# Performance work log

Hardware: AMD Instinct MI355X
Metric: run time of the kernel (lower is better)

Reference implementation:

```python
import jax, jax.numpy as jnp
import numpy as np

N_NODES = 100000

def _sage_conv(x, src, dst, W_l, b_l, W_r):
    # PyG SAGEConv (aggr='mean'): out = lin_l(mean_{j in N(i)} x_j) + lin_r(x_i)
    msg = x[src]                                             # [E, d] gather
    agg = jax.ops.segment_sum(msg, dst, num_segments=N_NODES)  # [N, d]
    deg = jax.ops.segment_sum(jnp.ones((src.shape[0],), x.dtype), dst,
                              num_segments=N_NODES)          # [N]
    mean = agg / jnp.maximum(deg, 1.0)[:, None]
    return mean @ W_l + b_l + x @ W_r

def setup_inputs() -> dict:
    key = jax.random.key(0)
    ks = jax.random.split(key, 8)
    d_in, d_hid, d_out = 128, 128, 64
    E = 1_600_000
    x = jax.random.normal(ks[0], (N_NODES, d_in), dtype=jnp.float32)
    edge_index = jax.random.randint(ks[1], (2, E), 0, N_NODES, dtype=jnp.int64)
    s1 = 1.0 / np.sqrt(d_in)
    s2 = 1.0 / np.sqrt(d_hid)
    return {
        "x": x,
        "W1_l": jax.random.uniform(ks[2], (d_in, d_hid), jnp.float32, -s1, s1),
        "b1":   jnp.zeros((d_hid,), jnp.float32),
        "W1_r": jax.random.uniform(ks[3], (d_in, d_hid), jnp.float32, -s1, s1),
        "W2_l": jax.random.uniform(ks[4], (d_hid, d_out), jnp.float32, -s2, s2),
        "b2":   jnp.zeros((d_out,), jnp.float32),
        "W2_r": jax.random.uniform(ks[5], (d_hid, d_out), jnp.float32, -s2, s2),
        "edge_index": edge_index,
    }

def reference(x, W1_l, b1, W1_r, W2_l, b2, W2_r, edge_index):
    src, dst = edge_index[0], edge_index[1]
    h = _sage_conv(x, src, dst, W1_l, b1, W1_r)
    h = jax.nn.relu(h)
    # dropout is identity in eval mode (p=0.5 train-only); omitted for determinism
    out = _sage_conv(h, src, dst, W2_l, b2, W2_r)
    return out
```

## Files before the change

### kernel.cpp

```cpp
#include <hip/hip_runtime.h>
#include <hip/hip_bf16.h>
#include <cstdint>


typedef __bf16 bf16x8 __attribute__((ext_vector_type(8)));
typedef float f32x4 __attribute__((ext_vector_type(4)));
typedef float f32x2 __attribute__((ext_vector_type(2)));

#define MAXBUCK 400
#define MAXEPT 16
#define HISTB 512
#define P2B 512
#define HSTRIDE 136

__device__ __forceinline__ unsigned short f2bf(float f) {
    union { float f; unsigned int u; } v; v.f = f;
    unsigned int u = v.u;
    unsigned int r = ((u >> 16) & 1u) + 0x7fffu;
    return (unsigned short)((u + r) >> 16);
}

__device__ __forceinline__ f32x2 up2(unsigned int u) {
    uint2 t; t.x = u << 16; t.y = u & 0xffff0000u;
    return __builtin_bit_cast(f32x2, t);
}
__device__ __forceinline__ void accp(const uint4& v, f32x2* a) {
    a[0] += up2(v.x);
    a[1] += up2(v.y);
    a[2] += up2(v.z);
    a[3] += up2(v.w);
}
__device__ __forceinline__ void accpw(const uint4& v, float w, f32x2* a) {
    a[0] += up2(v.x) * w;
    a[1] += up2(v.y) * w;
    a[2] += up2(v.z) * w;
    a[3] += up2(v.w) * w;
}

__device__ __forceinline__ int edge_val(const int* ei32, const long long* ei64,
                                        int is64, size_t idx) {
    return is64 ? (int)ei64[idx] : ei32[idx];
}

__global__ __launch_bounds__(256) void detect_zero(const void* ei, int n_nodes,
                                                   int* flag, int* bucket_cnt) {
    for (int i = threadIdx.x; i < MAXBUCK; i += 256) bucket_cnt[i] = 0;
    if (threadIdx.x == 0) {
        const long long* p = (const long long*)ei;
        int ok = 1;
        for (int i = 0; i < 8; ++i) {
            long long v = p[i];
            if (v < 0 || v >= n_nodes) ok = 0;
        }
        *flag = ok;
    }
}

__global__ __launch_bounds__(256) void prep_kernel(const float* __restrict__ x,
                                                   unsigned short* __restrict__ xb,
                                                   long long n8, int ncvt,
                                                   const float* __restrict__ W1l,
                                                   const float* __restrict__ W1r,
                                                   uint4* __restrict__ w1frag,
                                                   const float* __restrict__ W2l,
                                                   const float* __restrict__ W2r,
                                                   uint4* __restrict__ w2frag,
                                                   const int* ei32, const long long* ei64,
                                                   const int* flag, int E, int nbuck,
                                                   int* bucket_cnt) {
    int b = blockIdx.x;
    if (b < ncvt) {
        long long i = (long long)b * 256 + threadIdx.x;
        if (i >= n8) return;
        const float4* p = (const float4*)(x + i * 8);
        float4 a = p[0], c = p[1];
        uint4 o;
        o.x = (unsigned)f2bf(a.x) | ((unsigned)f2bf(a.y) << 16);
        o.y = (unsigned)f2bf(a.z) | ((unsigned)f2bf(a.w) << 16);
        o.z = (unsigned)f2bf(c.x) | ((unsigned)f2bf(c.y) << 16);
        o.w = (unsigned)f2bf(c.z) | ((unsigned)f2bf(c.w) << 16);
        ((uint4*)(xb))[i] = o;
        return;
    }
    if (b < ncvt + 16) {
        int tid = (b - ncvt) * 256 + threadIdx.x;
        int fi = tid >> 6, lane = tid & 63;
        int ct = fi >> 3, ks = fi & 7;
        int k0 = ks * 32 + (lane >> 4) * 8;
        int n = ct * 16 + (lane & 15);
        unsigned short e[8];
#pragma unroll
        for (int j = 0; j < 8; ++j) {
            int k = k0 + j;
            float v = (k < 128) ? W1l[k * 128 + n] : W1r[(k - 128) * 128 + n];
            e[j] = f2bf(v);
        }
        uint4 o;
        o.x = (unsigned)e[0] | ((unsigned)e[1] << 16);
        o.y = (unsigned)e[2] | ((unsigned)e[3] << 16);
        o.z = (unsigned)e[4] | ((unsigned)e[5] << 16);
        o.w = (unsigned)e[6] | ((unsigned)e[7] << 16);
        w1frag[tid] = o;
        return;
    }
    if (b < ncvt + 16 + 8) {
        int tid = (b - ncvt - 16) * 256 + threadIdx.x;
        int fi = tid >> 6, lane = tid & 63;
        int ct = fi >> 2, ks = fi & 3;
        int k0 = ks * 32 + (lane >> 4) * 8;
        int n = ct * 16 + (lane & 15);
        unsigned short e[8];
#pragma unroll
        for (int j = 0; j < 8; ++j) {
            int k = k0 + j;
            float v = (n < 64) ? W2l[k * 64 + n] : W2r[k * 64 + (n - 64)];
            e[j] = f2bf(v);
        }
        uint4 o;
        o.x = (unsigned)e[0] | ((unsigned)e[1] << 16);
        o.y = (unsigned)e[2] | ((unsigned)e[3] << 16);
        o.z = (unsigned)e[4] | ((unsigned)e[5] << 16);
        o.w = (unsigned)e[6] | ((unsigned)e[7] << 16);
        w2frag[tid] = o;
        return;
    }
    __shared__ int lhist[MAXBUCK];
    for (int i = threadIdx.x; i < nbuck; i += 256) lhist[i] = 0;
    __syncthreads();
    int is64 = *flag;
    int hb = b - (ncvt + 24);
    int stride = HISTB * 256;
    for (int e = hb * 256 + threadIdx.x; e < E; e += stride) {
        int d = edge_val(ei32, ei64, is64, (size_t)E + e);
        atomicAdd(&lhist[d >> 8], 1);
    }
    __syncthreads();
    for (int i = threadIdx.x; i < nbuck; i += 256) {
        int c = lhist[i];
        if (c) atomicAdd(&bucket_cnt[i], c);
    }
}

__global__ __launch_bounds__(256) void bucket_scan(const int* bucket_cnt, int nbuck,
                                                   int* bucket_base, int* bucket_pos) {
    int t = threadIdx.x;
    int i0 = 2 * t, i1 = 2 * t + 1;
    int a0 = (i0 < nbuck) ? bucket_cnt[i0] : 0;
    int a1 = (i1 < nbuck) ? bucket_cnt[i1] : 0;
    int tsum = a0 + a1;
    __shared__ int sc[256];
    sc[t] = tsum;
    __syncthreads();
    for (int o = 1; o < 256; o <<= 1) {
        int x = (t >= o) ? sc[t - o] : 0;
        __syncthreads();
        if (t >= o) sc[t] += x;
        __syncthreads();
    }
    int excl = sc[t] - tsum;
    if (i0 <= nbuck) { bucket_base[i0] = excl; if (i0 < nbuck) bucket_pos[i0] = excl; }
    if (i1 <= nbuck) { bucket_base[i1] = excl + a0; if (i1 < nbuck) bucket_pos[i1] = excl + a0; }
    if (t == 255) bucket_base[nbuck] = sc[255];
}

__global__ __launch_bounds__(256) void pass2_partition(const int* ei32, const long long* ei64,
                                                       const int* flag, int E, int ept,
                                                       int nbuck, int* bucket_pos,
                                                       unsigned* ebuf) {
    __shared__ int lhist[MAXBUCK];
    __shared__ int gbase[MAXBUCK];
    for (int i = threadIdx.x; i < nbuck; i += 256) lhist[i] = 0;
    __syncthreads();
    int is64 = *flag;
    int base_e = blockIdx.x * (ept * 256);
    unsigned ed[MAXEPT];
    int bidx[MAXEPT];
    int slot[MAXEPT];
#pragma unroll 4
    for (int i = 0; i < ept; ++i) {
        int e = base_e + i * 256 + threadIdx.x;
        if (e < E) {
            int s = edge_val(ei32, ei64, is64, (size_t)e);
            int d = edge_val(ei32, ei64, is64, (size_t)E + e);
            ed[i] = ((unsigned)s << 8) | (unsigned)(d & 255);
            bidx[i] = d >> 8;
            slot[i] = atomicAdd(&lhist[d >> 8], 1);
        } else {
            slot[i] = -1;
        }
    }
    __syncthreads();
    for (int i = threadIdx.x; i < nbuck; i += 256) {
        int c = lhist[i];
        gbase[i] = c ? atomicAdd(&bucket_pos[i], c) : 0;
    }
    __syncthreads();
#pragma unroll 4
    for (int i = 0; i < ept; ++i) {
        if (slot[i] >= 0) {
            ebuf[gbase[bidx[i]] + slot[i]] = ed[i];
        }
    }
}

__global__ __launch_bounds__(256) void pass3_finalize(const unsigned* __restrict__ ebuf,
                                                      const int* __restrict__ bucket_base,
                                                      int nbuck, int N, int E,
                                                      int* __restrict__ off,
                                                      int* __restrict__ csr) {
    __shared__ int lcnt[256];
    __shared__ int lexcl[256];
    __shared__ int sc[256];
    int b = blockIdx.x;
    int t = threadIdx.x;
    int d0 = b << 8;
    int nb = N - d0; if (nb > 256) nb = 256;
    int base = bucket_base[b];
    int m = bucket_base[b + 1] - base;

    lcnt[t] = 0;
    __syncthreads();
    for (int j = t; j < m; j += 256) {
        int li = (int)(ebuf[base + j] & 255u);
        atomicAdd(&lcnt[li], 1);
    }
    __syncthreads();
    int v = lcnt[t];
    sc[t] = v;
    __syncthreads();
    for (int o = 1; o < 256; o <<= 1) {
        int x = (t >= o) ? sc[t - o] : 0;
        __syncthreads();
        if (t >= o) sc[t] += x;
        __syncthreads();
    }
    int excl = sc[t] - v;
    lexcl[t] = excl;
    if (t < nb) off[d0 + t] = base + excl;
    if (b == nbuck - 1 && t == 0) off[N] = E;
    lcnt[t] = 0;
    __syncthreads();
    for (int j = t; j < m; j += 256) {
        unsigned ed = ebuf[base + j];
        int li = (int)(ed & 255u);
        int slot = atomicAdd(&lcnt[li], 1);
        csr[base + lexcl[li] + slot] = (int)(ed >> 8);
    }
}

__global__ __launch_bounds__(256) void agg_mean128_bf(const unsigned short* __restrict__ Xb,
                                                      const int* __restrict__ off,
                                                      const int* __restrict__ csr,
                                                      unsigned short* __restrict__ outb,
                                                      int n_nodes) {
    int node = blockIdx.x * 4 + (threadIdx.x >> 6);
    if (node >= n_nodes) return;
    int lane = threadIdx.x & 63;
    int quad = lane >> 4;
    int l16 = lane & 15;
    int s0 = off[node], s1 = off[node + 1];
    int deg = s1 - s0;
    f32x2 A0[4], A1[4];
#pragma unroll
    for (int k = 0; k < 4; ++k) { A0[k] = (f32x2){0.f, 0.f}; A1[k] = (f32x2){0.f, 0.f}; }
    int j = s0;
    for (; j + 8 <= s1; j += 8) {
        int p0 = csr[j + quad];
        int p1 = csr[j + 4 + quad];
        uint4 v0 = ((const uint4*)(Xb + (size_t)p0 * 128))[l16];
        uint4 v1 = ((const uint4*)(Xb + (size_t)p1 * 128))[l16];
        accp(v0, A0);
        accp(v1, A1);
    }
    if (j + 4 <= s1) {
        int p = csr[j + quad];
        uint4 v = ((const uint4*)(Xb + (size_t)p * 128))[l16];
        accp(v, A0);
        j += 4;
    }
    if (j < s1) {
        int jj = j + quad;
        int p = csr[(jj < s1) ? jj : (s1 - 1)];
        float w = (jj < s1) ? 1.0f : 0.0f;
        uint4 v = ((const uint4*)(Xb + (size_t)p * 128))[l16];
        accpw(v, w, A1);
    }
    float r[8];
#pragma unroll
    for (int k = 0; k < 4; ++k) {
        f32x2 s = A0[k] + A1[k];
        r[2 * k] = s.x;
        r[2 * k + 1] = s.y;
    }
#pragma unroll
    for (int k = 0; k < 8; ++k) r[k] += __shfl(r[k], lane ^ 16);
#pragma unroll
    for (int k = 0; k < 8; ++k) r[k] += __shfl(r[k], lane ^ 32);
    float inv = (deg > 0) ? 1.0f / (float)deg : 0.0f;
    if (quad == 0) {
        uint4 o;
        o.x = (unsigned)f2bf(r[0] * inv) | ((unsigned)f2bf(r[1] * inv) << 16);
        o.y = (unsigned)f2bf(r[2] * inv) | ((unsigned)f2bf(r[3] * inv) << 16);
        o.z = (unsigned)f2bf(r[4] * inv) | ((unsigned)f2bf(r[5] * inv) << 16);
        o.w = (unsigned)f2bf(r[6] * inv) | ((unsigned)f2bf(r[7] * inv) << 16);
        ((uint4*)(outb + (size_t)node * 128))[l16] = o;
    }
}

__global__ __launch_bounds__(256) void agg_mean64_bf_ep(const unsigned short* __restrict__ Zb,
                                                        const float* __restrict__ Wadd,
                                                        const int* __restrict__ off,
                                                        const int* __restrict__ csr,
                                                        float* __restrict__ out,
                                                        int n_nodes) {
    int node = blockIdx.x * 4 + (threadIdx.x >> 6);
    if (node >= n_nodes) return;
    int lane = threadIdx.x & 63;
    int oct = lane >> 3;
    int l8 = lane & 7;
    int s0 = off[node], s1 = off[node + 1];
    int deg = s1 - s0;
    f32x2 A0[4], A1[4];
#pragma unroll
    for (int k = 0; k < 4; ++k) { A0[k] = (f32x2){0.f, 0.f}; A1[k] = (f32x2){0.f, 0.f}; }
    int j = s0;
    for (; j + 16 <= s1; j += 16) {
        int p0 = csr[j + oct];
        int p1 = csr[j + 8 + oct];
        uint4 v0 = ((const uint4*)(Zb + (size_t)p0 * 64))[l8];
        uint4 v1 = ((const uint4*)(Zb + (size_t)p1 * 64))[l8];
        accp(v0, A0);
        accp(v1, A1);
    }
    if (j + 8 <= s1) {
        int p = csr[j + oct];
        uint4 v = ((const uint4*)(Zb + (size_t)p * 64))[l8];
        accp(v, A0);
        j += 8;
    }
    if (j < s1) {
        int jj = j + oct;
        int p = csr[(jj < s1) ? jj : (s1 - 1)];
        float w = (jj < s1) ? 1.0f : 0.0f;
        uint4 v = ((const uint4*)(Zb + (size_t)p * 64))[l8];
        accpw(v, w, A1);
    }
    float r[8];
#pragma unroll
    for (int k = 0; k < 4; ++k) {
        f32x2 s = A0[k] + A1[k];
        r[2 * k] = s.x;
        r[2 * k + 1] = s.y;
    }
#pragma unroll
    for (int k = 0; k < 8; ++k) r[k] += __shfl(r[k], lane ^ 8);
#pragma unroll
    for (int k = 0; k < 8; ++k) r[k] += __shfl(r[k], lane ^ 16);
#pragma unroll
    for (int k = 0; k < 8; ++k) r[k] += __shfl(r[k], lane ^ 32);
    float inv = (deg > 0) ? 1.0f / (float)deg : 0.0f;
    if (oct == 0) {
        const float4* wp = (const float4*)(Wadd + (size_t)node * 64 + l8 * 8);
        float4 w0 = wp[0], w1 = wp[1];
        float4 o0, o1;
        o0.x = r[0] * inv + w0.x; o0.y = r[1] * inv + w0.y;
        o0.z = r[2] * inv + w0.z; o0.w = r[3] * inv + w0.w;
        o1.x = r[4] * inv + w1.x; o1.y = r[5] * inv + w1.y;
        o1.z = r[6] * inv + w1.z; o1.w = r[7] * inv + w1.w;
        float4* op = (float4*)(out + (size_t)node * 64 + l8 * 8);
        op[0] = o0; op[1] = o1;
    }
}

__global__ __launch_bounds__(256, 3) void gemm12_mfma(const unsigned short* __restrict__ meanb,
                                                      const unsigned short* __restrict__ xb,
                                                      const uint4* __restrict__ w1frag,
                                                      const uint4* __restrict__ w2frag,
                                                      const float* __restrict__ b1,
                                                      const float* __restrict__ b2,
                                                      unsigned short* __restrict__ z2,
                                                      float* __restrict__ w2out,
                                                      int nrows) {
    __shared__ uint4 sW2[2048];
    __shared__ unsigned short hs[4][16 * HSTRIDE];
    for (int i = threadIdx.x; i < 2048; i += 256) sW2[i] = w2frag[i];
    __syncthreads();
    const int wid = threadIdx.x >> 6, lane = threadIdx.x & 63;
    const int quad = lane >> 4, l16 = lane & 15;
    const int m0 = blockIdx.x * 128 + wid * 32;
    unsigned short* hsw = &hs[wid][0];
    const uint4* w1p = w1frag + lane;

#pragma unroll
    for (int mt = 0; mt < 2; ++mt) {
        int row = m0 + mt * 16 + l16;
        int rowc = (row < nrows) ? row : (nrows - 1);
        const uint4* mrow = (const uint4*)(meanb + (size_t)rowc * 128);
        const uint4* xrow = (const uint4*)(xb + (size_t)rowc * 128);
        bf16x8 af[8];
#pragma unroll
        for (int ks = 0; ks < 4; ++ks) {
            af[ks]     = __builtin_bit_cast(bf16x8, mrow[ks * 4 + quad]);
            af[ks + 4] = __builtin_bit_cast(bf16x8, xrow[ks * 4 + quad]);
        }

#pragma unroll
        for (int ct = 0; ct < 8; ++ct) {
            f32x4 acc = (f32x4){0.f, 0.f, 0.f, 0.f};
#pragma unroll
            for (int ks = 0; ks < 8; ++ks) {
                bf16x8 bf = __builtin_bit_cast(bf16x8, w1p[(ct * 8 + ks) * 64]);
                acc = __builtin_amdgcn_mfma_f32_16x16x32_bf16(af[ks], bf, acc, 0, 0, 0);
            }
            int col = ct * 16 + l16;
            float bb = b1[col];
#pragma unroll
            for (int r = 0; r < 4; ++r) {
                float v = fmaxf(acc[r] + bb, 0.f);
                hs[wid][(quad * 4 + r) * HSTRIDE + col] = f2bf(v);
            }
        }

        bf16x8 af2[4];
#pragma unroll
        for (int ks = 0; ks < 4; ++ks) {
            uint4 t = *(const uint4*)(hsw + l16 * HSTRIDE + ks * 32 + quad * 8);
            af2[ks] = __builtin_bit_cast(bf16x8, t);
        }

#pragma unroll
        for (int ct = 0; ct < 8; ++ct) {
            f32x4 acc = (f32x4){0.f, 0.f, 0.f, 0.f};
#pragma unroll
            for (int ks = 0; ks < 4; ++ks) {
                bf16x8 bf = __builtin_bit_cast(bf16x8, sW2[(ct * 4 + ks) * 64 + lane]);
                acc = __builtin_amdgcn_mfma_f32_16x16x32_bf16(af2[ks], bf, acc, 0, 0, 0);
            }
            int col = ct * 16 + l16;
#pragma unroll
            for (int r = 0; r < 4; ++r) {
                int orow = m0 + mt * 16 + quad * 4 + r;
                if (orow < nrows) {
                    if (col < 64) {
                        z2[(size_t)orow * 64 + col] = f2bf(acc[r]);
                    } else {
                        w2out[(size_t)orow * 64 + (col - 64)] = acc[r] + b2[col - 64];
                    }
                }
            }
        }
    }
}

extern "C" void kernel_launch(void* const* d_in, const int* in_sizes, int n_in,
                              void* d_out, int out_size, void* d_ws, size_t ws_size,
                              hipStream_t stream) {
    const float* x    = (const float*)d_in[0];
    const float* W1_l = (const float*)d_in[1];
    const float* b1   = (const float*)d_in[2];
    const float* W1_r = (const float*)d_in[3];
    const float* W2_l = (const float*)d_in[4];
    const float* b2   = (const float*)d_in[5];
    const float* W2_r = (const float*)d_in[6];
    const void*  ei   = d_in[7];
    float* out = (float*)d_out;

    const int N = in_sizes[0] / 128;
    const int E = in_sizes[7] / 2;
    const int nbuck = (N + 255) >> 8;

    uintptr_t base = (uintptr_t)d_ws;
    int* flag = (int*)base;
    int* bucket_cnt  = (int*)(base + 64);
    int* bucket_base = bucket_cnt + MAXBUCK;
    int* bucket_pos  = bucket_base + MAXBUCK + 1;
    int* off = (int*)(base + 4096 + 3 * MAXBUCK * 4);
    off = (int*)(((uintptr_t)off + 255) & ~(uintptr_t)255);
    int* csr = off + (N + 1);
    uintptr_t p = ((uintptr_t)(csr + E) + 255) & ~(uintptr_t)255;
    unsigned short* xb    = (unsigned short*)p; p += (size_t)N * 128 * 2;
    unsigned short* meanb = (unsigned short*)p; p += (size_t)N * 128 * 2;
    unsigned short* hbr   = (unsigned short*)p; p += (size_t)N * 128 * 2;
    uint4* w1frag = (uint4*)p; p += 4096 * 16;
    uint4* w2frag = (uint4*)p; p += 2048 * 16;
    unsigned* ebuf = (unsigned*)meanb;
    unsigned short* z2 = hbr;
    float* w2 = (float*)xb;

    const int* ei32 = (const int*)ei;
    const long long* ei64 = (const long long*)ei;

    detect_zero<<<1, 256, 0, stream>>>(ei, N, flag, bucket_cnt);

    long long n8 = (long long)N * 128 / 8;
    int ncvt = (int)((n8 + 255) / 256);
    prep_kernel<<<ncvt + 16 + 8 + HISTB, 256, 0, stream>>>(
        x, xb, n8, ncvt, W1_l, W1_r, w1frag, W2_l, W2_r, w2frag,
        ei32, ei64, flag, E, nbuck, bucket_cnt);

    bucket_scan<<<1, 256, 0, stream>>>(bucket_cnt, nbuck, bucket_base, bucket_pos);
    int ept = (E + P2B * 256 - 1) / (P2B * 256);
    pass2_partition<<<P2B, 256, 0, stream>>>(ei32, ei64, flag, E, ept, nbuck,
                                             bucket_pos, ebuf);
    pass3_finalize<<<nbuck, 256, 0, stream>>>(ebuf, bucket_base, nbuck, N, E, off, csr);

    int ablocks = (N + 3) / 4;
    int gblocks = (N + 127) / 128;

    agg_mean128_bf<<<ablocks, 256, 0, stream>>>(xb, off, csr, meanb, N);
    gemm12_mfma<<<gblocks, 256, 0, stream>>>(meanb, xb, w1frag, w2frag, b1, b2,
                                             z2, w2, N);
    agg_mean64_bf_ep<<<ablocks, 256, 0, stream>>>(z2, w2, off, csr, out, N);
}
```

Measured before the change: 319.2 us.

## Store bf16 features in column-slab layout for cache-local layer-1 aggregation

Converts x into eight column slabs of 16 bf16 features per node. The layer-1 mean aggregation then runs slice by slice, each slice being a 3.2MB table that can stay in cache, with two lanes per node. The GEMM reads its A fragments from the slab layout, and w2 gets its own workspace buffer instead of aliasing xb, which is now still needed. The cost is eight passes over the CSR indices and divergent per-node loops, since lanes whose node has a smaller degree sit idle until the wave's largest degree finishes.

```diff
diff --git a/kernel.cpp b/kernel.cpp
--- a/kernel.cpp
+++ b/kernel.cpp
@@ -57,8 +57,8 @@
 }
 
 __global__ __launch_bounds__(256) void prep_kernel(const float* __restrict__ x,
-                                                   unsigned short* __restrict__ xb,
-                                                   long long n8, int ncvt,
+                                                   unsigned short* __restrict__ xslab,
+                                                   int N, int ncvt,
                                                    const float* __restrict__ W1l,
                                                    const float* __restrict__ W1r,
                                                    uint4* __restrict__ w1frag,
@@ -70,16 +70,22 @@
                                                    int* bucket_cnt) {
     int b = blockIdx.x;
     if (b < ncvt) {
-        long long i = (long long)b * 256 + threadIdx.x;
-        if (i >= n8) return;
-        const float4* p = (const float4*)(x + i * 8);
-        float4 a = p[0], c = p[1];
-        uint4 o;
-        o.x = (unsigned)f2bf(a.x) | ((unsigned)f2bf(a.y) << 16);
-        o.y = (unsigned)f2bf(a.z) | ((unsigned)f2bf(a.w) << 16);
-        o.z = (unsigned)f2bf(c.x) | ((unsigned)f2bf(c.y) << 16);
-        o.w = (unsigned)f2bf(c.z) | ((unsigned)f2bf(c.w) << 16);
-        ((uint4*)(xb))[i] = o;
+        int nl = threadIdx.x >> 3, s = threadIdx.x & 7;
+        int node = b * 32 + nl;
+        if (node >= N) return;
+        const float4* px = (const float4*)(x + (size_t)node * 128 + s * 16);
+        float4 a0 = px[0], a1 = px[1], a2 = px[2], a3 = px[3];
+        uint4 o0, o1;
+        o0.x = (unsigned)f2bf(a0.x) | ((unsigned)f2bf(a0.y) << 16);
+        o0.y = (unsigned)f2bf(a0.z) | ((unsigned)f2bf(a0.w) << 16);
+        o0.z = (unsigned)f2bf(a1.x) | ((unsigned)f2bf(a1.y) << 16);
+        o0.w = (unsigned)f2bf(a1.z) | ((unsigned)f2bf(a1.w) << 16);
+        o1.x = (unsigned)f2bf(a2.x) | ((unsigned)f2bf(a2.y) << 16);
+        o1.y = (unsigned)f2bf(a2.z) | ((unsigned)f2bf(a2.w) << 16);
+        o1.z = (unsigned)f2bf(a3.x) | ((unsigned)f2bf(a3.y) << 16);
+        o1.w = (unsigned)f2bf(a3.z) | ((unsigned)f2bf(a3.w) << 16);
+        uint4* dst = (uint4*)(xslab + (size_t)s * N * 16 + (size_t)node * 16);
+        dst[0] = o0; dst[1] = o1;
         return;
     }
     if (b < ncvt + 16) {
@@ -248,62 +254,40 @@
     }
 }
 
-__global__ __launch_bounds__(256) void agg_mean128_bf(const unsigned short* __restrict__ Xb,
-                                                      const int* __restrict__ off,
-                                                      const int* __restrict__ csr,
-                                                      unsigned short* __restrict__ outb,
-                                                      int n_nodes) {
-    int node = blockIdx.x * 4 + (threadIdx.x >> 6);
-    if (node >= n_nodes) return;
-    int lane = threadIdx.x & 63;
-    int quad = lane >> 4;
-    int l16 = lane & 15;
-    int s0 = off[node], s1 = off[node + 1];
-    int deg = s1 - s0;
-    f32x2 A0[4], A1[4];
-#pragma unroll
-    for (int k = 0; k < 4; ++k) { A0[k] = (f32x2){0.f, 0.f}; A1[k] = (f32x2){0.f, 0.f}; }
-    int j = s0;
-    for (; j + 8 <= s1; j += 8) {
-        int p0 = csr[j + quad];
-        int p1 = csr[j + 4 + quad];
-        uint4 v0 = ((const uint4*)(Xb + (size_t)p0 * 128))[l16];
-        uint4 v1 = ((const uint4*)(Xb + (size_t)p1 * 128))[l16];
-        accp(v0, A0);
-        accp(v1, A1);
-    }
-    if (j + 4 <= s1) {
-        int p = csr[j + quad];
-        uint4 v = ((const uint4*)(Xb + (size_t)p * 128))[l16];
-        accp(v, A0);
-        j += 4;
-    }
-    if (j < s1) {
-        int jj = j + quad;
-        int p = csr[(jj < s1) ? jj : (s1 - 1)];
-        float w = (jj < s1) ? 1.0f : 0.0f;
-        uint4 v = ((const uint4*)(Xb + (size_t)p * 128))[l16];
-        accpw(v, w, A1);
-    }
-    float r[8];
-#pragma unroll
-    for (int k = 0; k < 4; ++k) {
-        f32x2 s = A0[k] + A1[k];
-        r[2 * k] = s.x;
-        r[2 * k + 1] = s.y;
-    }
-#pragma unroll
-    for (int k = 0; k < 8; ++k) r[k] += __shfl(r[k], lane ^ 16);
-#pragma unroll
-    for (int k = 0; k < 8; ++k) r[k] += __shfl(r[k], lane ^ 32);
-    float inv = (deg > 0) ? 1.0f / (float)deg : 0.0f;
-    if (quad == 0) {
+__global__ __launch_bounds__(256) void agg_mean128_slab(const unsigned short* __restrict__ xslab,
+                                                        const int* __restrict__ off,
+                                                        const int* __restrict__ csr,
+                                                        unsigned short* __restrict__ meanslab,
+                                                        int N) {
+    int slice = blockIdx.x & 7;
+    int g = blockIdx.x >> 3;
+    int wid = threadIdx.x >> 6, lane = threadIdx.x & 63;
+    int nl = lane >> 1, h = lane & 1;
+    int node = g * 128 + wid * 32 + nl;
+    int valid = node < N;
+    int s0 = 0, deg = 0;
+    if (valid) { s0 = off[node]; deg = off[node + 1] - s0; }
+    const unsigned short* slab = xslab + (size_t)slice * N * 16 + h * 8;
+    f32x2 A[4];
+    A[0] = A[1] = A[2] = A[3] = (f32x2){0.f, 0.f};
+    for (int i = 0; ; ++i) {
+        int act = (i < deg);
+        if (!__any(act)) break;
+        if (act) {
+            int p = csr[s0 + i];
+            uint4 v = *(const uint4*)(slab + (size_t)p * 16);
+            accp(v, A);
+        }
+    }
+    if (valid) {
+        float inv = (deg > 0) ? 1.0f / (float)deg : 0.0f;
+        f32x2 r0 = A[0] * inv, r1 = A[1] * inv, r2 = A[2] * inv, r3 = A[3] * inv;
         uint4 o;
-        o.x = (unsigned)f2bf(r[0] * inv) | ((unsigned)f2bf(r[1] * inv) << 16);
-        o.y = (unsigned)f2bf(r[2] * inv) | ((unsigned)f2bf(r[3] * inv) << 16);
-        o.z = (unsigned)f2bf(r[4] * inv) | ((unsigned)f2bf(r[5] * inv) << 16);
-        o.w = (unsigned)f2bf(r[6] * inv) | ((unsigned)f2bf(r[7] * inv) << 16);
-        ((uint4*)(outb + (size_t)node * 128))[l16] = o;
+        o.x = (unsigned)f2bf(r0.x) | ((unsigned)f2bf(r0.y) << 16);
+        o.y = (unsigned)f2bf(r1.x) | ((unsigned)f2bf(r1.y) << 16);
+        o.z = (unsigned)f2bf(r2.x) | ((unsigned)f2bf(r2.y) << 16);
+        o.w = (unsigned)f2bf(r3.x) | ((unsigned)f2bf(r3.y) << 16);
+        *(uint4*)(meanslab + (size_t)slice * N * 16 + (size_t)node * 16 + h * 8) = o;
     }
 }
 
@@ -372,8 +356,8 @@
     }
 }
 
-__global__ __launch_bounds__(256, 3) void gemm12_mfma(const unsigned short* __restrict__ meanb,
-                                                      const unsigned short* __restrict__ xb,
+__global__ __launch_bounds__(256, 3) void gemm12_mfma(const unsigned short* __restrict__ meanslab,
+                                                      const unsigned short* __restrict__ xslab,
                                                       const uint4* __restrict__ w1frag,
                                                       const uint4* __restrict__ w2frag,
                                                       const float* __restrict__ b1,
@@ -390,18 +374,21 @@
     const int m0 = blockIdx.x * 128 + wid * 32;
     unsigned short* hsw = &hs[wid][0];
     const uint4* w1p = w1frag + lane;
+    const size_t sstride = (size_t)nrows * 16;
+    const int eo = (quad & 1) * 8;
+    const int slq = quad >> 1;
 
 #pragma unroll
     for (int mt = 0; mt < 2; ++mt) {
         int row = m0 + mt * 16 + l16;
         int rowc = (row < nrows) ? row : (nrows - 1);
-        const uint4* mrow = (const uint4*)(meanb + (size_t)rowc * 128);
-        const uint4* xrow = (const uint4*)(xb + (size_t)rowc * 128);
         bf16x8 af[8];
 #pragma unroll
         for (int ks = 0; ks < 4; ++ks) {
-            af[ks]     = __builtin_bit_cast(bf16x8, mrow[ks * 4 + quad]);
-            af[ks + 4] = __builtin_bit_cast(bf16x8, xrow[ks * 4 + quad]);
+            af[ks]     = __builtin_bit_cast(bf16x8,
+                *(const uint4*)(meanslab + (size_t)(2 * ks + slq) * sstride + (size_t)rowc * 16 + eo));
+            af[ks + 4] = __builtin_bit_cast(bf16x8,
+                *(const uint4*)(xslab + (size_t)(2 * ks + slq) * sstride + (size_t)rowc * 16 + eo));
         }
 
 #pragma unroll
@@ -478,24 +465,23 @@
     off = (int*)(((uintptr_t)off + 255) & ~(uintptr_t)255);
     int* csr = off + (N + 1);
     uintptr_t p = ((uintptr_t)(csr + E) + 255) & ~(uintptr_t)255;
-    unsigned short* xb    = (unsigned short*)p; p += (size_t)N * 128 * 2;
-    unsigned short* meanb = (unsigned short*)p; p += (size_t)N * 128 * 2;
-    unsigned short* hbr   = (unsigned short*)p; p += (size_t)N * 128 * 2;
+    unsigned short* xslab    = (unsigned short*)p; p += (size_t)N * 128 * 2;
+    unsigned short* meanslab = (unsigned short*)p; p += (size_t)N * 128 * 2;
+    unsigned short* hbr      = (unsigned short*)p; p += (size_t)N * 128 * 2;
     uint4* w1frag = (uint4*)p; p += 4096 * 16;
     uint4* w2frag = (uint4*)p; p += 2048 * 16;
-    unsigned* ebuf = (unsigned*)meanb;
+    float* w2 = (float*)p; p += (size_t)N * 64 * 4;
+    unsigned* ebuf = (unsigned*)meanslab;
     unsigned short* z2 = hbr;
-    float* w2 = (float*)xb;
 
     const int* ei32 = (const int*)ei;
     const long long* ei64 = (const long long*)ei;
 
     detect_zero<<<1, 256, 0, stream>>>(ei, N, flag, bucket_cnt);
 
-    long long n8 = (long long)N * 128 / 8;
-    int ncvt = (int)((n8 + 255) / 256);
+    int ncvt = (N + 31) / 32;
     prep_kernel<<<ncvt + 16 + 8 + HISTB, 256, 0, stream>>>(
-        x, xb, n8, ncvt, W1_l, W1_r, w1frag, W2_l, W2_r, w2frag,
+        x, xslab, N, ncvt, W1_l, W1_r, w1frag, W2_l, W2_r, w2frag,
         ei32, ei64, flag, E, nbuck, bucket_cnt);
 
     bucket_scan<<<1, 256, 0, stream>>>(bucket_cnt, nbuck, bucket_base, bucket_pos);
@@ -504,11 +490,12 @@
                                              bucket_pos, ebuf);
     pass3_finalize<<<nbuck, 256, 0, stream>>>(ebuf, bucket_base, nbuck, N, E, off, csr);
 
+    int gblocks = (N + 127) / 128;
+    int aslab_blocks = gblocks * 8;
     int ablocks = (N + 3) / 4;
-    int gblocks = (N + 127) / 128;
-
-    agg_mean128_bf<<<ablocks, 256, 0, stream>>>(xb, off, csr, meanb, N);
-    gemm12_mfma<<<gblocks, 256, 0, stream>>>(meanb, xb, w1frag, w2frag, b1, b2,
+
+    agg_mean128_slab<<<aslab_blocks, 256, 0, stream>>>(xslab, off, csr, meanslab, N);
+    gemm12_mfma<<<gblocks, 256, 0, stream>>>(meanslab, xslab, w1frag, w2frag, b1, b2,
                                              z2, w2, N);
     agg_mean64_bf_ep<<<ablocks, 256, 0, stream>>>(z2, w2, off, csr, out, N);
 }
```

Measured after the change: 386.3 us. 21.0% more time.

## Share weight fragments across two row tiles and drop LDS staging of W2

Applied to the files above, without the earlier changes.

Rebuilds the fused two-layer GEMM so each wave loads both 16-row tiles first, then runs every weight fragment through two MFMAs, one per tile. This halves the weight fragment loads per output. W2 fragments now come from global memory or cache instead of a shared-memory copy, which removes the LDS fill and block barrier, and the launch bound is raised to four blocks per SM. The w2 output also gets its own workspace region instead of aliasing xb, which avoids a write-after-read hazard but uses more workspace and may add register pressure.

```diff
diff --git a/kernel.cpp b/kernel.cpp
--- a/kernel.cpp
+++ b/kernel.cpp
@@ -372,7 +372,7 @@
     }
 }
 
-__global__ __launch_bounds__(256, 3) void gemm12_mfma(const unsigned short* __restrict__ meanb,
+__global__ __launch_bounds__(256, 4) void gemm12_mfma(const unsigned short* __restrict__ meanb,
                                                       const unsigned short* __restrict__ xb,
                                                       const uint4* __restrict__ w1frag,
                                                       const uint4* __restrict__ w2frag,
@@ -381,62 +381,70 @@
                                                       unsigned short* __restrict__ z2,
                                                       float* __restrict__ w2out,
                                                       int nrows) {
-    __shared__ uint4 sW2[2048];
-    __shared__ unsigned short hs[4][16 * HSTRIDE];
-    for (int i = threadIdx.x; i < 2048; i += 256) sW2[i] = w2frag[i];
-    __syncthreads();
+    __shared__ unsigned short hs[4][32 * HSTRIDE];
     const int wid = threadIdx.x >> 6, lane = threadIdx.x & 63;
     const int quad = lane >> 4, l16 = lane & 15;
     const int m0 = blockIdx.x * 128 + wid * 32;
     unsigned short* hsw = &hs[wid][0];
     const uint4* w1p = w1frag + lane;
-
+    const uint4* w2p = w2frag + lane;
+
+    bf16x8 af[2][8];
 #pragma unroll
     for (int mt = 0; mt < 2; ++mt) {
         int row = m0 + mt * 16 + l16;
         int rowc = (row < nrows) ? row : (nrows - 1);
         const uint4* mrow = (const uint4*)(meanb + (size_t)rowc * 128);
         const uint4* xrow = (const uint4*)(xb + (size_t)rowc * 128);
-        bf16x8 af[8];
 #pragma unroll
         for (int ks = 0; ks < 4; ++ks) {
-            af[ks]     = __builtin_bit_cast(bf16x8, mrow[ks * 4 + quad]);
-            af[ks + 4] = __builtin_bit_cast(bf16x8, xrow[ks * 4 + quad]);
-        }
-
-#pragma unroll
-        for (int ct = 0; ct < 8; ++ct) {
-            f32x4 acc = (f32x4){0.f, 0.f, 0.f, 0.f};
-#pragma unroll
-            for (int ks = 0; ks < 8; ++ks) {
-                bf16x8 bf = __builtin_bit_cast(bf16x8, w1p[(ct * 8 + ks) * 64]);
-                acc = __builtin_amdgcn_mfma_f32_16x16x32_bf16(af[ks], bf, acc, 0, 0, 0);
-            }
-            int col = ct * 16 + l16;
-            float bb = b1[col];
-#pragma unroll
-            for (int r = 0; r < 4; ++r) {
-                float v = fmaxf(acc[r] + bb, 0.f);
-                hs[wid][(quad * 4 + r) * HSTRIDE + col] = f2bf(v);
-            }
-        }
-
-        bf16x8 af2[4];
+            af[mt][ks]     = __builtin_bit_cast(bf16x8, mrow[ks * 4 + quad]);
+            af[mt][ks + 4] = __builtin_bit_cast(bf16x8, xrow[ks * 4 + quad]);
+        }
+    }
+
+#pragma unroll
+    for (int ct = 0; ct < 8; ++ct) {
+        f32x4 a0 = (f32x4){0.f, 0.f, 0.f, 0.f};
+        f32x4 a1 = (f32x4){0.f, 0.f, 0.f, 0.f};
+#pragma unroll
+        for (int ks = 0; ks < 8; ++ks) {
+            bf16x8 bf = __builtin_bit_cast(bf16x8, w1p[(ct * 8 + ks) * 64]);
+            a0 = __builtin_amdgcn_mfma_f32_16x16x32_bf16(af[0][ks], bf, a0, 0, 0, 0);
+            a1 = __builtin_amdgcn_mfma_f32_16x16x32_bf16(af[1][ks], bf, a1, 0, 0, 0);
+        }
+        int col = ct * 16 + l16;
+        float bb = b1[col];
+#pragma unroll
+        for (int r = 0; r < 4; ++r) {
+            hsw[(quad * 4 + r) * HSTRIDE + col] = f2bf(fmaxf(a0[r] + bb, 0.f));
+            hsw[(16 + quad * 4 + r) * HSTRIDE + col] = f2bf(fmaxf(a1[r] + bb, 0.f));
+        }
+    }
+
+    bf16x8 af2[2][4];
+#pragma unroll
+    for (int mt = 0; mt < 2; ++mt)
 #pragma unroll
         for (int ks = 0; ks < 4; ++ks) {
-            uint4 t = *(const uint4*)(hsw + l16 * HSTRIDE + ks * 32 + quad * 8);
-            af2[ks] = __builtin_bit_cast(bf16x8, t);
-        }
-
-#pragma unroll
-        for (int ct = 0; ct < 8; ++ct) {
-            f32x4 acc = (f32x4){0.f, 0.f, 0.f, 0.f};
-#pragma unroll
-            for (int ks = 0; ks < 4; ++ks) {
-                bf16x8 bf = __builtin_bit_cast(bf16x8, sW2[(ct * 4 + ks) * 64 + lane]);
-                acc = __builtin_amdgcn_mfma_f32_16x16x32_bf16(af2[ks], bf, acc, 0, 0, 0);
-            }
-            int col = ct * 16 + l16;
+            uint4 t = *(const uint4*)(hsw + (mt * 16 + l16) * HSTRIDE + ks * 32 + quad * 8);
+            af2[mt][ks] = __builtin_bit_cast(bf16x8, t);
+        }
+
+#pragma unroll
+    for (int ct = 0; ct < 8; ++ct) {
+        f32x4 a0 = (f32x4){0.f, 0.f, 0.f, 0.f};
+        f32x4 a1 = (f32x4){0.f, 0.f, 0.f, 0.f};
+#pragma unroll
+        for (int ks = 0; ks < 4; ++ks) {
+            bf16x8 bf = __builtin_bit_cast(bf16x8, w2p[(ct * 4 + ks) * 64]);
+            a0 = __builtin_amdgcn_mfma_f32_16x16x32_bf16(af2[0][ks], bf, a0, 0, 0, 0);
+            a1 = __builtin_amdgcn_mfma_f32_16x16x32_bf16(af2[1][ks], bf, a1, 0, 0, 0);
+        }
+        int col = ct * 16 + l16;
+#pragma unroll
+        for (int mt = 0; mt < 2; ++mt) {
+            f32x4 acc = mt ? a1 : a0;
 #pragma unroll
             for (int r = 0; r < 4; ++r) {
                 int orow = m0 + mt * 16 + quad * 4 + r;
@@ -483,9 +491,9 @@
     unsigned short* hbr   = (unsigned short*)p; p += (size_t)N * 128 * 2;
     uint4* w1frag = (uint4*)p; p += 4096 * 16;
     uint4* w2frag = (uint4*)p; p += 2048 * 16;
+    float* w2 = (float*)p; p += (size_t)N * 64 * 4;
     unsigned* ebuf = (unsigned*)meanb;
     unsigned short* z2 = hbr;
-    float* w2 = (float*)xb;
 
     const int* ei32 = (const int*)ei;
     const long long* ei64 = (const long long*)ei;
```

After: 305.6 us. 4.3% less time.
